# Optimization experiments

Measured on AMD Instinct MI355X. Metric: run time of the kernel, lower is better.

## Reference

```python
import jax, jax.numpy as jnp
import numpy as np

D = 1024      # d_model
H = 16        # heads
DH = D // H   # d_per_head = 64
E = 2         # expand_ratio
EPS = 1e-10


def _ln(x, g, b, eps=1e-5):
    mu = jnp.mean(x, axis=-1, keepdims=True)
    var = jnp.mean((x - mu) ** 2, axis=-1, keepdims=True)
    return (x - mu) / jnp.sqrt(var + eps) * g + b


def setup_inputs() -> dict:
    key = jax.random.key(0)
    ks = jax.random.split(key, 12)

    def w(k, fan_in, shape):
        return jax.random.normal(k, shape, jnp.float32) * (1.0 / np.sqrt(fan_in))

    return {
        "x": jax.random.normal(ks[0], (8, 1024, D), jnp.float32),
        "w_qvk": w(ks[1], D, (D, 3 * D)), "b_qvk": jnp.zeros((3 * D,), jnp.float32),
        "w_q": w(ks[2], D, (D, D)), "b_q": jnp.zeros((D,), jnp.float32),
        "w_k": w(ks[3], D, (D, D)), "b_k": jnp.zeros((D,), jnp.float32),
        "w_v": w(ks[4], D, (D, D)), "b_v": jnp.zeros((D,), jnp.float32),
        "w_o": w(ks[5], D, (D, D)), "b_o": jnp.zeros((D,), jnp.float32),
        "ln1_g": jnp.ones((D,), jnp.float32), "ln1_b": jnp.zeros((D,), jnp.float32),
        "w1": w(ks[6], D, (D, E * D)), "b1": jnp.zeros((E * D,), jnp.float32),
        "w2": w(ks[7], E * D, (E * D, D)), "b2": jnp.zeros((D,), jnp.float32),
        "ln2_g": jnp.ones((D,), jnp.float32), "ln2_b": jnp.zeros((D,), jnp.float32),
    }


def reference(x, w_qvk, b_qvk, w_q, b_q, w_k, b_k, w_v, b_v, w_o, b_o,
              ln1_g, ln1_b, w1, b1, w2, b2, ln2_g, ln2_b):
    n, m, _ = x.shape
    qvk = x @ w_qvk + b_qvk                       # [n, m, 3D]
    q = qvk[..., 0:D] @ w_q + b_q
    k = qvk[..., D:2 * D] @ w_k + b_k
    v = qvk[..., 2 * D:3 * D] @ w_v + b_v
    # NOTE: original rearranges '(d h)' with h=head -> head is the INNER factor
    q = q.reshape(n, m, DH, H)
    k = k.reshape(n, m, DH, H)
    v = v.reshape(n, m, DH, H)
    scores = jnp.einsum('nqdh,nkdh->nhqk', q, k) / (np.sqrt(DH) + EPS)
    p = jax.nn.softmax(scores, axis=-1)           # [n, h, q, k]
    vh = jnp.einsum('nkdh,nhqk->nhqd', v, p)      # [n, h, q, d]
    vh = vh.transpose(0, 2, 1, 3).reshape(n, m, D)  # 'n h q d -> n q (h d)'
    att = _ln(vh @ w_o + b_o, ln1_g, ln1_b)
    hidden = jnp.clip(att @ w1 + b1, 0.0, 6.0)    # ReLU6
    out = hidden @ w2 + b2
    return _ln(out, ln2_g, ln2_b)
```

## Files before the change

kernel.cpp:

```cpp
#include <hip/hip_runtime.h>
#include <math.h>


#define D_MODEL 1024
#define SEQ     1024
#define NHEAD   16

typedef short          s16x8 __attribute__((ext_vector_type(8)));
typedef unsigned short u16x4 __attribute__((ext_vector_type(4)));
typedef float          f32x4 __attribute__((ext_vector_type(4)));

__device__ __forceinline__ unsigned short f2bf(float f) {
    union { float f; unsigned u; } c; c.f = f;
    unsigned u = c.u;
    return (unsigned short)((u + 0x7FFFu + ((u >> 16) & 1u)) >> 16);
}
__device__ __forceinline__ float bf2f(unsigned short h) {
    union { unsigned u; float f; } c; c.u = ((unsigned)h) << 16; return c.f;
}

#define GLB(p) ((const __attribute__((address_space(1))) void*)(p))
#define LDSP(p) ((__attribute__((address_space(3))) void*)(p))

__global__ __launch_bounds__(256) void cast_f32_bf16(
    const float* __restrict__ in, unsigned short* __restrict__ out, int n4)
{
    int i = blockIdx.x * 256 + threadIdx.x;
    if (i < n4) {
        float4 v = ((const float4*)in)[i];
        u16x4 o;
        o[0] = f2bf(v.x); o[1] = f2bf(v.y); o[2] = f2bf(v.z); o[3] = f2bf(v.w);
        ((u16x4*)out)[i] = o;
    }
}

template <bool PERM>
__global__ __launch_bounds__(256) void wt_cast(
    const float* __restrict__ W, unsigned short* __restrict__ Wt, int K, int N)
{
    __shared__ float T[32][33];
    const int tx = threadIdx.x, ty = threadIdx.y;
    const int nb = blockIdx.x * 32, kb = blockIdx.y * 32;
    const int nOut = nb + tx;
    const int nSrc = PERM ? (((nOut & 63) << 4) + (nOut >> 6)) : nOut;
#pragma unroll
    for (int q = 0; q < 4; ++q)
        T[ty + q * 8][tx] = W[(size_t)(kb + ty + q * 8) * N + nSrc];
    __syncthreads();
#pragma unroll
    for (int q = 0; q < 4; ++q)
        Wt[(size_t)(nb + ty + q * 8) * K + kb + tx] = f2bf(T[tx][ty + q * 8]);
}

__global__ void perm_bias(const float* __restrict__ in, float* __restrict__ out)
{
    int i = threadIdx.x;
    out[i] = in[((i & 63) << 4) + (i >> 6)];
}

__global__ __launch_bounds__(256) void transpose_v(
    const unsigned short* __restrict__ vb, unsigned short* __restrict__ vt, int M)
{
    const int T = blockIdx.x * 256 + threadIdx.x;
    const int c  = T & 1023;
    const int r0 = (T >> 10) << 3;
    s16x8 o;
#pragma unroll
    for (int i = 0; i < 8; ++i)
        o[i] = (short)vb[(size_t)(r0 + i) * 1024 + c];
    *(s16x8*)&vt[(size_t)c * M + r0] = o;
}

template <int ACT>
__global__ __launch_bounds__(256) void gemm_bf16(
    const unsigned short* __restrict__ A, int lda,
    const unsigned short* __restrict__ Bt,
    const float* __restrict__ bias,
    unsigned short* __restrict__ C, int ldc,
    int M, int N, int K)
{
    __shared__ unsigned short At[128 * 32];
    __shared__ unsigned short Bl[128 * 32];
    const int tid = threadIdx.x;
    const int w = tid >> 6, l = tid & 63, g = l >> 4, lr = l & 15;
    const int row0 = blockIdx.y * 128, col0 = blockIdx.x * 128;
    const int wr = (w >> 1) * 64, wc = (w & 1) * 64;

    f32x4 zero = {0.f, 0.f, 0.f, 0.f};
    f32x4 acc[4][4];
#pragma unroll
    for (int m = 0; m < 4; ++m)
#pragma unroll
        for (int n = 0; n < 4; ++n) acc[m][n] = zero;

    const int srow = w * 32 + (l >> 2);
    const int scol = (l & 3) * 8;
    const unsigned short* aS = A + (size_t)(row0 + srow) * lda + scol;
    const unsigned short* bS = Bt + (size_t)(col0 + srow) * K + scol;
    unsigned short* aD0 = &At[w * 1024];
    unsigned short* aD1 = &At[w * 1024 + 512];
    unsigned short* bD0 = &Bl[w * 1024];
    unsigned short* bD1 = &Bl[w * 1024 + 512];

    for (int k0 = 0; k0 < K; k0 += 32) {
        __syncthreads();
        __builtin_amdgcn_global_load_lds(GLB(aS + k0), LDSP(aD0), 16, 0, 0);
        __builtin_amdgcn_global_load_lds(GLB(aS + (size_t)16 * lda + k0), LDSP(aD1), 16, 0, 0);
        __builtin_amdgcn_global_load_lds(GLB(bS + k0), LDSP(bD0), 16, 0, 0);
        __builtin_amdgcn_global_load_lds(GLB(bS + (size_t)16 * K + k0), LDSP(bD1), 16, 0, 0);
        __syncthreads();

        s16x8 a[4], b[4];
#pragma unroll
        for (int m = 0; m < 4; ++m)
            a[m] = *(const s16x8*)&At[(wr + m * 16 + lr) * 32 + g * 8];
#pragma unroll
        for (int n = 0; n < 4; ++n)
            b[n] = *(const s16x8*)&Bl[(wc + n * 16 + lr) * 32 + g * 8];
#pragma unroll
        for (int m = 0; m < 4; ++m)
#pragma unroll
            for (int n = 0; n < 4; ++n)
                acc[m][n] = __builtin_amdgcn_mfma_f32_16x16x32_bf16(
                    a[m], b[n], acc[m][n], 0, 0, 0);
    }

    float bv[4];
#pragma unroll
    for (int n = 0; n < 4; ++n) bv[n] = bias[col0 + wc + n * 16 + lr];
#pragma unroll
    for (int m = 0; m < 4; ++m)
#pragma unroll
        for (int n = 0; n < 4; ++n)
#pragma unroll
            for (int r = 0; r < 4; ++r) {
                float vv = acc[m][n][r] + bv[n];
                if (ACT == 1) vv = fminf(fmaxf(vv, 0.f), 6.f);
                const int row = row0 + wr + m * 16 + g * 4 + r;
                const int col = col0 + wc + n * 16 + lr;
                C[(size_t)row * ldc + col] = f2bf(vv);
            }
}

__global__ __launch_bounds__(256) void attn_mfma(
    const unsigned short* __restrict__ q,
    const unsigned short* __restrict__ k,
    const unsigned short* __restrict__ vt,
    unsigned short* __restrict__ vh, int M)
{
    __shared__ unsigned short Kt[64 * 64];
    __shared__ unsigned short Vl[64 * 64];
    __shared__ unsigned short Pt[4][16 * 64];

    const int tid = threadIdx.x, w = tid >> 6, l = tid & 63;
    const int g = l >> 4, lr = l & 15;
    const int qt = blockIdx.x, h = blockIdx.y, nb = blockIdx.z;

    const unsigned short* qB = q + (size_t)nb * SEQ * D_MODEL + h * 64;
    const unsigned short* kB = k + (size_t)nb * SEQ * D_MODEL + h * 64;
    const unsigned short* vB = vt + (size_t)h * 64 * M + nb * SEQ;

    s16x8 qa0, qa1;
    {
        const unsigned short* qp = qB + (size_t)(qt * 64 + w * 16 + lr) * D_MODEL + g * 8;
        qa0 = *(const s16x8*)qp;
        qa1 = *(const s16x8*)(qp + 32);
    }

    f32x4 zero = {0.f, 0.f, 0.f, 0.f};
    f32x4 Oc[4];
#pragma unroll
    for (int nd = 0; nd < 4; ++nd) Oc[nd] = zero;
    float mrun[4], lrun[4];
#pragma unroll
    for (int r = 0; r < 4; ++r) { mrun[r] = -3.0e38f; lrun[r] = 0.f; }

    const int srow = w * 16 + (l >> 3);
    const int scol = (((l & 7) * 16) ^ (((l >> 3) & 7) << 4)) >> 1;

    for (int kt = 0; kt < 16; ++kt) {
        __syncthreads();
        const unsigned short* ks0 = kB + (size_t)(kt * 64 + srow) * D_MODEL + scol;
        __builtin_amdgcn_global_load_lds(GLB(ks0), LDSP(&Kt[w * 1024]), 16, 0, 0);
        __builtin_amdgcn_global_load_lds(GLB(ks0 + (size_t)8 * D_MODEL),
                                         LDSP(&Kt[w * 1024 + 512]), 16, 0, 0);
        const unsigned short* vs0 = vB + (size_t)srow * M + kt * 64 + scol;
        __builtin_amdgcn_global_load_lds(GLB(vs0), LDSP(&Vl[w * 1024]), 16, 0, 0);
        __builtin_amdgcn_global_load_lds(GLB(vs0 + (size_t)8 * M),
                                         LDSP(&Vl[w * 1024 + 512]), 16, 0, 0);
        __syncthreads();

        f32x4 sc[4];
#pragma unroll
        for (int nk = 0; nk < 4; ++nk) {
            const int row = nk * 16 + lr;
            const int swz = (row & 7) << 4;
            const s16x8 b0 = *(const s16x8*)&Kt[row * 64 + (((g * 16) ^ swz) >> 1)];
            const s16x8 b1 = *(const s16x8*)&Kt[row * 64 + (((g * 16 + 64) ^ swz) >> 1)];
            sc[nk] = __builtin_amdgcn_mfma_f32_16x16x32_bf16(qa0, b0, zero, 0, 0, 0);
            sc[nk] = __builtin_amdgcn_mfma_f32_16x16x32_bf16(qa1, b1, sc[nk], 0, 0, 0);
        }

        float corr[4];
#pragma unroll
        for (int r = 0; r < 4; ++r) {
            float s0 = sc[0][r] * 0.125f, s1 = sc[1][r] * 0.125f;
            float s2 = sc[2][r] * 0.125f, s3 = sc[3][r] * 0.125f;
            float mt = fmaxf(fmaxf(s0, s1), fmaxf(s2, s3));
            mt = fmaxf(mt, __shfl_xor(mt, 1, 64));
            mt = fmaxf(mt, __shfl_xor(mt, 2, 64));
            mt = fmaxf(mt, __shfl_xor(mt, 4, 64));
            mt = fmaxf(mt, __shfl_xor(mt, 8, 64));
            const float mn = fmaxf(mrun[r], mt);
            corr[r] = __expf(mrun[r] - mn);
            mrun[r] = mn;
            float p0 = __expf(s0 - mn), p1 = __expf(s1 - mn);
            float p2 = __expf(s2 - mn), p3 = __expf(s3 - mn);
            float ps = p0 + p1 + p2 + p3;
            ps += __shfl_xor(ps, 1, 64);
            ps += __shfl_xor(ps, 2, 64);
            ps += __shfl_xor(ps, 4, 64);
            ps += __shfl_xor(ps, 8, 64);
            lrun[r] = lrun[r] * corr[r] + ps;

            const int qrow = g * 4 + r;
            const int pswz = (qrow & 7) << 4;
            Pt[w][qrow * 64 + (((2 * (0 * 16 + lr)) ^ pswz) >> 1)] = f2bf(p0);
            Pt[w][qrow * 64 + (((2 * (1 * 16 + lr)) ^ pswz) >> 1)] = f2bf(p1);
            Pt[w][qrow * 64 + (((2 * (2 * 16 + lr)) ^ pswz) >> 1)] = f2bf(p2);
            Pt[w][qrow * 64 + (((2 * (3 * 16 + lr)) ^ pswz) >> 1)] = f2bf(p3);
        }
#pragma unroll
        for (int nd = 0; nd < 4; ++nd)
#pragma unroll
            for (int r = 0; r < 4; ++r) Oc[nd][r] *= corr[r];

#pragma unroll
        for (int kk = 0; kk < 2; ++kk) {
            const int prswz = (lr & 7) << 4;
            const s16x8 pa = *(const s16x8*)
                &Pt[w][lr * 64 + (((g * 16 + kk * 64) ^ prswz) >> 1)];
#pragma unroll
            for (int nd = 0; nd < 4; ++nd) {
                const int row = nd * 16 + lr;
                const int vswz = (row & 7) << 4;
                const s16x8 bv = *(const s16x8*)
                    &Vl[row * 64 + (((g * 16 + kk * 64) ^ vswz) >> 1)];
                Oc[nd] = __builtin_amdgcn_mfma_f32_16x16x32_bf16(pa, bv, Oc[nd], 0, 0, 0);
            }
        }
    }

    float inv[4];
#pragma unroll
    for (int r = 0; r < 4; ++r) inv[r] = 1.0f / lrun[r];
#pragma unroll
    for (int nd = 0; nd < 4; ++nd)
#pragma unroll
        for (int r = 0; r < 4; ++r) {
            const int qrow = g * 4 + r;
            const int pswz = (qrow & 7) << 4;
            Pt[w][qrow * 64 + (((2 * (nd * 16 + lr)) ^ pswz) >> 1)] =
                f2bf(Oc[nd][r] * inv[r]);
        }
    const int rr = l >> 2;
    unsigned short* dst = vh + (size_t)(nb * SEQ + qt * 64 + w * 16 + rr) * D_MODEL + h * 64;
#pragma unroll
    for (int hh = 0; hh < 2; ++hh) {
        const int sb = (l & 3) * 32 + hh * 16;
        s16x8 o = *(const s16x8*)&Pt[w][rr * 64 + ((sb ^ ((rr & 7) << 4)) >> 1)];
        *(s16x8*)(dst + (sb >> 1)) = o;
    }
}

template <int OUTF32>
__global__ __launch_bounds__(256) void ln_bf16(
    const unsigned short* __restrict__ x,
    const float* __restrict__ gg,
    const float* __restrict__ bb,
    void* __restrict__ outp)
{
    const int row = blockIdx.x, tid = threadIdx.x;
    u16x4 xv = *(const u16x4*)&x[(size_t)row * 1024 + tid * 4];
    float f0 = bf2f(xv[0]), f1 = bf2f(xv[1]), f2 = bf2f(xv[2]), f3 = bf2f(xv[3]);
    float s  = f0 + f1 + f2 + f3;
    float sq = f0 * f0 + f1 * f1 + f2 * f2 + f3 * f3;
#pragma unroll
    for (int off = 1; off < 64; off <<= 1) {
        s  += __shfl_xor(s,  off, 64);
        sq += __shfl_xor(sq, off, 64);
    }
    __shared__ float ls[4], lq[4];
    const int wave = tid >> 6;
    if ((tid & 63) == 0) { ls[wave] = s; lq[wave] = sq; }
    __syncthreads();
    s  = ls[0] + ls[1] + ls[2] + ls[3];
    sq = lq[0] + lq[1] + lq[2] + lq[3];
    const float mu  = s * (1.0f / 1024.0f);
    const float var = sq * (1.0f / 1024.0f) - mu * mu;
    const float rs  = rsqrtf(var + 1e-5f);
    const float4 gv = ((const float4*)gg)[tid];
    const float4 bv = ((const float4*)bb)[tid];
    float o0 = (f0 - mu) * rs * gv.x + bv.x;
    float o1 = (f1 - mu) * rs * gv.y + bv.y;
    float o2 = (f2 - mu) * rs * gv.z + bv.z;
    float o3 = (f3 - mu) * rs * gv.w + bv.w;
    if (OUTF32) {
        float4 o; o.x = o0; o.y = o1; o.z = o2; o.w = o3;
        ((float4*)outp)[(size_t)row * 256 + tid] = o;
    } else {
        u16x4 o;
        o[0] = f2bf(o0); o[1] = f2bf(o1); o[2] = f2bf(o2); o[3] = f2bf(o3);
        ((u16x4*)outp)[(size_t)row * 256 + tid] = o;
    }
}

extern "C" void kernel_launch(void* const* d_in, const int* in_sizes, int n_in,
                              void* d_out, int out_size, void* d_ws, size_t ws_size,
                              hipStream_t stream)
{
    const float* x     = (const float*)d_in[0];
    const float* w_qvk = (const float*)d_in[1];
    const float* b_qvk = (const float*)d_in[2];
    const float* w_q   = (const float*)d_in[3];
    const float* b_q   = (const float*)d_in[4];
    const float* w_k   = (const float*)d_in[5];
    const float* b_k   = (const float*)d_in[6];
    const float* w_v   = (const float*)d_in[7];
    const float* b_v   = (const float*)d_in[8];
    const float* w_o   = (const float*)d_in[9];
    const float* b_o   = (const float*)d_in[10];
    const float* ln1_g = (const float*)d_in[11];
    const float* ln1_b = (const float*)d_in[12];
    const float* w1    = (const float*)d_in[13];
    const float* b1    = (const float*)d_in[14];
    const float* w2    = (const float*)d_in[15];
    const float* b2    = (const float*)d_in[16];
    const float* ln2_g = (const float*)d_in[17];
    const float* ln2_b = (const float*)d_in[18];
    float* out = (float*)d_out;

    const int nbatch = in_sizes[0] / (SEQ * D_MODEL);
    const int M = nbatch * SEQ;

    char* ws = (char*)d_ws;
    size_t off = 0;
    auto alloc = [&](size_t bytes) { size_t o = off; off += (bytes + 255) & ~(size_t)255; return o; };
    const size_t XB   = alloc((size_t)M * 1024 * 2);
    const size_t WQVK = alloc((size_t)3072 * 1024 * 2);
    const size_t WQ   = alloc((size_t)1024 * 1024 * 2);
    const size_t WK   = alloc((size_t)1024 * 1024 * 2);
    const size_t WV   = alloc((size_t)1024 * 1024 * 2);
    const size_t WO   = alloc((size_t)1024 * 1024 * 2);
    const size_t W1   = alloc((size_t)2048 * 1024 * 2);
    const size_t W2   = alloc((size_t)2048 * 1024 * 2);
    const size_t BQP  = alloc(4096);
    const size_t BKP  = alloc(4096);
    const size_t BVP  = alloc(4096);
    const size_t QVKB = alloc((size_t)M * 3072 * 2);
    const size_t QBUF = alloc((size_t)M * 1024 * 2);
    const size_t KBUF = alloc((size_t)M * 1024 * 2);
    const size_t VBUF = alloc((size_t)M * 1024 * 2);
    const size_t VT   = alloc((size_t)M * 1024 * 2);
    const size_t VH   = QVKB;
    const size_t ATTP = QVKB + (size_t)M * 1024 * 2;
    const size_t ATT  = QVKB + (size_t)M * 2048 * 2;
    const size_t HID  = QBUF;
    const size_t OUTP = VBUF;

    unsigned short* xb   = (unsigned short*)(ws + XB);
    unsigned short* wqvk = (unsigned short*)(ws + WQVK);
    unsigned short* wq   = (unsigned short*)(ws + WQ);
    unsigned short* wk   = (unsigned short*)(ws + WK);
    unsigned short* wv   = (unsigned short*)(ws + WV);
    unsigned short* wo   = (unsigned short*)(ws + WO);
    unsigned short* wt1  = (unsigned short*)(ws + W1);
    unsigned short* wt2  = (unsigned short*)(ws + W2);
    float*          bqp  = (float*)(ws + BQP);
    float*          bkp  = (float*)(ws + BKP);
    float*          bvp  = (float*)(ws + BVP);
    unsigned short* qvkb = (unsigned short*)(ws + QVKB);
    unsigned short* qb   = (unsigned short*)(ws + QBUF);
    unsigned short* kb   = (unsigned short*)(ws + KBUF);
    unsigned short* vb   = (unsigned short*)(ws + VBUF);
    unsigned short* vtb  = (unsigned short*)(ws + VT);
    unsigned short* vhb  = (unsigned short*)(ws + VH);
    unsigned short* attp = (unsigned short*)(ws + ATTP);
    unsigned short* attb = (unsigned short*)(ws + ATT);
    unsigned short* hid  = (unsigned short*)(ws + HID);
    unsigned short* outp = (unsigned short*)(ws + OUTP);

    const dim3 tb(32, 8);

    cast_f32_bf16<<<(M * 1024 / 4 + 255) / 256, 256, 0, stream>>>(x, xb, M * 1024 / 4);
    wt_cast<false><<<dim3(96, 32), tb, 0, stream>>>(w_qvk, wqvk, 1024, 3072);
    wt_cast<true ><<<dim3(32, 32), tb, 0, stream>>>(w_q, wq, 1024, 1024);
    wt_cast<true ><<<dim3(32, 32), tb, 0, stream>>>(w_k, wk, 1024, 1024);
    wt_cast<true ><<<dim3(32, 32), tb, 0, stream>>>(w_v, wv, 1024, 1024);
    wt_cast<false><<<dim3(32, 32), tb, 0, stream>>>(w_o, wo, 1024, 1024);
    wt_cast<false><<<dim3(64, 32), tb, 0, stream>>>(w1, wt1, 1024, 2048);
    wt_cast<false><<<dim3(32, 64), tb, 0, stream>>>(w2, wt2, 2048, 1024);
    perm_bias<<<1, 1024, 0, stream>>>(b_q, bqp);
    perm_bias<<<1, 1024, 0, stream>>>(b_k, bkp);
    perm_bias<<<1, 1024, 0, stream>>>(b_v, bvp);

    gemm_bf16<0><<<dim3(24, M / 128), 256, 0, stream>>>(
        xb, 1024, wqvk, b_qvk, qvkb, 3072, M, 3072, 1024);
    gemm_bf16<0><<<dim3(8, M / 128), 256, 0, stream>>>(
        qvkb + 0,    3072, wq, bqp, qb, 1024, M, 1024, 1024);
    gemm_bf16<0><<<dim3(8, M / 128), 256, 0, stream>>>(
        qvkb + 1024, 3072, wk, bkp, kb, 1024, M, 1024, 1024);
    gemm_bf16<0><<<dim3(8, M / 128), 256, 0, stream>>>(
        qvkb + 2048, 3072, wv, bvp, vb, 1024, M, 1024, 1024);

    transpose_v<<<(M / 8) * 1024 / 256, 256, 0, stream>>>(vb, vtb, M);
    attn_mfma<<<dim3(SEQ / 64, NHEAD, nbatch), 256, 0, stream>>>(qb, kb, vtb, vhb, M);

    gemm_bf16<0><<<dim3(8, M / 128), 256, 0, stream>>>(
        vhb, 1024, wo, b_o, attp, 1024, M, 1024, 1024);
    ln_bf16<0><<<M, 256, 0, stream>>>(attp, ln1_g, ln1_b, attb);

    gemm_bf16<1><<<dim3(16, M / 128), 256, 0, stream>>>(
        attb, 1024, wt1, b1, hid, 2048, M, 2048, 1024);
    gemm_bf16<0><<<dim3(8, M / 128), 256, 0, stream>>>(
        hid, 2048, wt2, b2, outp, 1024, M, 1024, 2048);
    ln_bf16<1><<<M, 256, 0, stream>>>(outp, ln2_g, ln2_b, out);
}
```

Before: 627.4 us.

## Fold chained QKV projections into combined weights and fold softmax scale

Precomputes the combined weight W_qvk_slice·W_q (and likewise for k and v) plus folded biases with a small weight-only MFMA GEMM, so activations pass through one 3072-wide GEMM instead of a QVK GEMM followed by three further 1024-wide GEMMs. The 1/sqrt(dh) scale is folded into the Q weights and bias, removing the per-score multiply in attention, and attention reads Q/K directly from the strided combined buffer. Softmax probabilities are converted with packed bf16 conversion instructions. This removes roughly 3 of 6 GFLOP-equivalents of activation GEMM work at the cost of a 3×1024³ weight GEMM per call and different rounding, since the combined weight is rounded to bf16 once.

```diff
diff --git a/kernel.cpp b/kernel.cpp
--- a/kernel.cpp
+++ b/kernel.cpp
@@ -52,14 +52,107 @@
         Wt[(size_t)(nb + ty + q * 8) * K + kb + tx] = f2bf(T[tx][ty + q * 8]);
 }
 
-__global__ void perm_bias(const float* __restrict__ in, float* __restrict__ out)
-{
-    int i = threadIdx.x;
-    out[i] = in[((i & 63) << 4) + (i >> 6)];
+__global__ __launch_bounds__(256) void bias_fold(
+    const float* __restrict__ bqvk,
+    const float* __restrict__ wq, const float* __restrict__ wk,
+    const float* __restrict__ wv,
+    const float* __restrict__ bq, const float* __restrict__ bk,
+    const float* __restrict__ bv,
+    float* __restrict__ bc)
+{
+    const int n  = blockIdx.x;
+    const int sl = blockIdx.y;
+    const float* w  = sl == 0 ? wq : sl == 1 ? wk : wv;
+    const float* bs = sl == 0 ? bq : sl == 1 ? bk : bv;
+    const int s = sl << 10;
+    const int nSrc = ((n & 63) << 4) + (n >> 6);
+    const int t = threadIdx.x;
+    float p = 0.f;
+    for (int k = t; k < 1024; k += 256)
+        p += bqvk[s + k] * w[(size_t)k * 1024 + nSrc];
+#pragma unroll
+    for (int off = 1; off < 64; off <<= 1) p += __shfl_xor(p, off, 64);
+    __shared__ float red[4];
+    if ((t & 63) == 0) red[t >> 6] = p;
+    __syncthreads();
+    if (t == 0) {
+        float dot = red[0] + red[1] + red[2] + red[3];
+        bc[s + n] = (dot + bs[nSrc]) * (sl == 0 ? 0.125f : 1.0f);
+    }
+}
+
+__global__ __launch_bounds__(256) void wcomb_mfma(
+    const unsigned short* __restrict__ Ws,
+    const unsigned short* __restrict__ Wb,
+    unsigned short* __restrict__ Wc)
+{
+    __shared__ unsigned short At[128 * 32];
+    __shared__ unsigned short Bl[128 * 32];
+    const int tid = threadIdx.x;
+    const int w = tid >> 6, l = tid & 63, g = l >> 4, lr = l & 15;
+    const int row0 = blockIdx.y * 128, col0 = blockIdx.x * 128;
+    const int z = blockIdx.z;
+    const int wr = (w >> 1) * 64, wcq = (w & 1) * 64;
+    const float scl = (z == 0) ? 0.125f : 1.0f;
+
+    const unsigned short* A  = Ws + (size_t)z * 1024 * 1024;
+    const unsigned short* Bt = Wb + z * 1024;
+    unsigned short*       C  = Wc + (size_t)z * 1024 * 1024;
+
+    f32x4 zero = {0.f, 0.f, 0.f, 0.f};
+    f32x4 acc[4][4];
+#pragma unroll
+    for (int m = 0; m < 4; ++m)
+#pragma unroll
+        for (int n = 0; n < 4; ++n) acc[m][n] = zero;
+
+    const int srow = w * 32 + (l >> 2);
+    const int scol = (l & 3) * 8;
+    const unsigned short* aS = A + (size_t)(row0 + srow) * 1024 + scol;
+    const unsigned short* bS = Bt + (size_t)(col0 + srow) * 3072 + scol;
+    unsigned short* aD0 = &At[w * 1024];
+    unsigned short* aD1 = &At[w * 1024 + 512];
+    unsigned short* bD0 = &Bl[w * 1024];
+    unsigned short* bD1 = &Bl[w * 1024 + 512];
+
+    for (int k0 = 0; k0 < 1024; k0 += 32) {
+        __syncthreads();
+        __builtin_amdgcn_global_load_lds(GLB(aS + k0), LDSP(aD0), 16, 0, 0);
+        __builtin_amdgcn_global_load_lds(GLB(aS + (size_t)16 * 1024 + k0), LDSP(aD1), 16, 0, 0);
+        __builtin_amdgcn_global_load_lds(GLB(bS + k0), LDSP(bD0), 16, 0, 0);
+        __builtin_amdgcn_global_load_lds(GLB(bS + (size_t)16 * 3072 + k0), LDSP(bD1), 16, 0, 0);
+        __syncthreads();
+
+        s16x8 a[4], b[4];
+#pragma unroll
+        for (int m = 0; m < 4; ++m)
+            a[m] = *(const s16x8*)&At[(wr + m * 16 + lr) * 32 + g * 8];
+#pragma unroll
+        for (int n = 0; n < 4; ++n)
+            b[n] = *(const s16x8*)&Bl[(wcq + n * 16 + lr) * 32 + g * 8];
+#pragma unroll
+        for (int m = 0; m < 4; ++m)
+#pragma unroll
+            for (int n = 0; n < 4; ++n)
+                acc[m][n] = __builtin_amdgcn_mfma_f32_16x16x32_bf16(
+                    a[m], b[n], acc[m][n], 0, 0, 0);
+    }
+
+#pragma unroll
+    for (int m = 0; m < 4; ++m)
+#pragma unroll
+        for (int n = 0; n < 4; ++n)
+#pragma unroll
+            for (int r = 0; r < 4; ++r) {
+                const int row = row0 + wr + m * 16 + g * 4 + r;
+                const int col = col0 + wcq + n * 16 + lr;
+                C[(size_t)row * 1024 + col] = f2bf(acc[m][n][r] * scl);
+            }
 }
 
 __global__ __launch_bounds__(256) void transpose_v(
-    const unsigned short* __restrict__ vb, unsigned short* __restrict__ vt, int M)
+    const unsigned short* __restrict__ vb, unsigned short* __restrict__ vt,
+    int M, int ldv)
 {
     const int T = blockIdx.x * 256 + threadIdx.x;
     const int c  = T & 1023;
@@ -67,7 +160,7 @@
     s16x8 o;
 #pragma unroll
     for (int i = 0; i < 8; ++i)
-        o[i] = (short)vb[(size_t)(r0 + i) * 1024 + c];
+        o[i] = (short)vb[(size_t)(r0 + i) * ldv + c];
     *(s16x8*)&vt[(size_t)c * M + r0] = o;
 }
 
@@ -143,10 +236,9 @@
 }
 
 __global__ __launch_bounds__(256) void attn_mfma(
-    const unsigned short* __restrict__ q,
-    const unsigned short* __restrict__ k,
+    const unsigned short* __restrict__ qkv,
     const unsigned short* __restrict__ vt,
-    unsigned short* __restrict__ vh, int M)
+    unsigned short* __restrict__ vh, int M, int ldq)
 {
     __shared__ unsigned short Kt[64 * 64];
     __shared__ unsigned short Vl[64 * 64];
@@ -156,13 +248,13 @@
     const int g = l >> 4, lr = l & 15;
     const int qt = blockIdx.x, h = blockIdx.y, nb = blockIdx.z;
 
-    const unsigned short* qB = q + (size_t)nb * SEQ * D_MODEL + h * 64;
-    const unsigned short* kB = k + (size_t)nb * SEQ * D_MODEL + h * 64;
+    const unsigned short* qB = qkv + (size_t)nb * SEQ * ldq + h * 64;
+    const unsigned short* kB = qkv + (size_t)nb * SEQ * ldq + 1024 + h * 64;
     const unsigned short* vB = vt + (size_t)h * 64 * M + nb * SEQ;
 
     s16x8 qa0, qa1;
     {
-        const unsigned short* qp = qB + (size_t)(qt * 64 + w * 16 + lr) * D_MODEL + g * 8;
+        const unsigned short* qp = qB + (size_t)(qt * 64 + w * 16 + lr) * ldq + g * 8;
         qa0 = *(const s16x8*)qp;
         qa1 = *(const s16x8*)(qp + 32);
     }
@@ -180,9 +272,9 @@
 
     for (int kt = 0; kt < 16; ++kt) {
         __syncthreads();
-        const unsigned short* ks0 = kB + (size_t)(kt * 64 + srow) * D_MODEL + scol;
+        const unsigned short* ks0 = kB + (size_t)(kt * 64 + srow) * ldq + scol;
         __builtin_amdgcn_global_load_lds(GLB(ks0), LDSP(&Kt[w * 1024]), 16, 0, 0);
-        __builtin_amdgcn_global_load_lds(GLB(ks0 + (size_t)8 * D_MODEL),
+        __builtin_amdgcn_global_load_lds(GLB(ks0 + (size_t)8 * ldq),
                                          LDSP(&Kt[w * 1024 + 512]), 16, 0, 0);
         const unsigned short* vs0 = vB + (size_t)srow * M + kt * 64 + scol;
         __builtin_amdgcn_global_load_lds(GLB(vs0), LDSP(&Vl[w * 1024]), 16, 0, 0);
@@ -204,8 +296,7 @@
         float corr[4];
 #pragma unroll
         for (int r = 0; r < 4; ++r) {
-            float s0 = sc[0][r] * 0.125f, s1 = sc[1][r] * 0.125f;
-            float s2 = sc[2][r] * 0.125f, s3 = sc[3][r] * 0.125f;
+            float s0 = sc[0][r], s1 = sc[1][r], s2 = sc[2][r], s3 = sc[3][r];
             float mt = fmaxf(fmaxf(s0, s1), fmaxf(s2, s3));
             mt = fmaxf(mt, __shfl_xor(mt, 1, 64));
             mt = fmaxf(mt, __shfl_xor(mt, 2, 64));
@@ -223,12 +314,15 @@
             ps += __shfl_xor(ps, 8, 64);
             lrun[r] = lrun[r] * corr[r] + ps;
 
+            unsigned pk01, pk23;
+            asm("v_cvt_pk_bf16_f32 %0, %1, %2" : "=v"(pk01) : "v"(p0), "v"(p1));
+            asm("v_cvt_pk_bf16_f32 %0, %1, %2" : "=v"(pk23) : "v"(p2), "v"(p3));
             const int qrow = g * 4 + r;
             const int pswz = (qrow & 7) << 4;
-            Pt[w][qrow * 64 + (((2 * (0 * 16 + lr)) ^ pswz) >> 1)] = f2bf(p0);
-            Pt[w][qrow * 64 + (((2 * (1 * 16 + lr)) ^ pswz) >> 1)] = f2bf(p1);
-            Pt[w][qrow * 64 + (((2 * (2 * 16 + lr)) ^ pswz) >> 1)] = f2bf(p2);
-            Pt[w][qrow * 64 + (((2 * (3 * 16 + lr)) ^ pswz) >> 1)] = f2bf(p3);
+            Pt[w][qrow * 64 + (((2 * (0 * 16 + lr)) ^ pswz) >> 1)] = (unsigned short)pk01;
+            Pt[w][qrow * 64 + (((2 * (1 * 16 + lr)) ^ pswz) >> 1)] = (unsigned short)(pk01 >> 16);
+            Pt[w][qrow * 64 + (((2 * (2 * 16 + lr)) ^ pswz) >> 1)] = (unsigned short)pk23;
+            Pt[w][qrow * 64 + (((2 * (3 * 16 + lr)) ^ pswz) >> 1)] = (unsigned short)(pk23 >> 16);
         }
 #pragma unroll
         for (int nd = 0; nd < 4; ++nd)
@@ -346,75 +440,57 @@
     char* ws = (char*)d_ws;
     size_t off = 0;
     auto alloc = [&](size_t bytes) { size_t o = off; off += (bytes + 255) & ~(size_t)255; return o; };
-    const size_t XB   = alloc((size_t)M * 1024 * 2);
-    const size_t WQVK = alloc((size_t)3072 * 1024 * 2);
-    const size_t WQ   = alloc((size_t)1024 * 1024 * 2);
-    const size_t WK   = alloc((size_t)1024 * 1024 * 2);
-    const size_t WV   = alloc((size_t)1024 * 1024 * 2);
-    const size_t WO   = alloc((size_t)1024 * 1024 * 2);
-    const size_t W1   = alloc((size_t)2048 * 1024 * 2);
-    const size_t W2   = alloc((size_t)2048 * 1024 * 2);
-    const size_t BQP  = alloc(4096);
-    const size_t BKP  = alloc(4096);
-    const size_t BVP  = alloc(4096);
-    const size_t QVKB = alloc((size_t)M * 3072 * 2);
-    const size_t QBUF = alloc((size_t)M * 1024 * 2);
-    const size_t KBUF = alloc((size_t)M * 1024 * 2);
-    const size_t VBUF = alloc((size_t)M * 1024 * 2);
-    const size_t VT   = alloc((size_t)M * 1024 * 2);
-    const size_t VH   = QVKB;
-    const size_t ATTP = QVKB + (size_t)M * 1024 * 2;
-    const size_t ATT  = QVKB + (size_t)M * 2048 * 2;
-    const size_t HID  = QBUF;
-    const size_t OUTP = VBUF;
-
-    unsigned short* xb   = (unsigned short*)(ws + XB);
-    unsigned short* wqvk = (unsigned short*)(ws + WQVK);
-    unsigned short* wq   = (unsigned short*)(ws + WQ);
-    unsigned short* wk   = (unsigned short*)(ws + WK);
-    unsigned short* wv   = (unsigned short*)(ws + WV);
-    unsigned short* wo   = (unsigned short*)(ws + WO);
-    unsigned short* wt1  = (unsigned short*)(ws + W1);
-    unsigned short* wt2  = (unsigned short*)(ws + W2);
-    float*          bqp  = (float*)(ws + BQP);
-    float*          bkp  = (float*)(ws + BKP);
-    float*          bvp  = (float*)(ws + BVP);
-    unsigned short* qvkb = (unsigned short*)(ws + QVKB);
-    unsigned short* qb   = (unsigned short*)(ws + QBUF);
-    unsigned short* kb   = (unsigned short*)(ws + KBUF);
-    unsigned short* vb   = (unsigned short*)(ws + VBUF);
-    unsigned short* vtb  = (unsigned short*)(ws + VT);
-    unsigned short* vhb  = (unsigned short*)(ws + VH);
-    unsigned short* attp = (unsigned short*)(ws + ATTP);
-    unsigned short* attb = (unsigned short*)(ws + ATT);
-    unsigned short* hid  = (unsigned short*)(ws + HID);
-    unsigned short* outp = (unsigned short*)(ws + OUTP);
+    const size_t XB    = alloc((size_t)M * 1024 * 2);
+    const size_t QKVB  = alloc((size_t)M * 3072 * 2);
+    const size_t VT    = alloc((size_t)M * 1024 * 2);
+    const size_t VH    = alloc((size_t)M * 1024 * 2);
+    const size_t WQVKB = alloc((size_t)1024 * 3072 * 2);
+    const size_t WSUB  = alloc((size_t)3 * 1024 * 1024 * 2);
+    const size_t WC    = alloc((size_t)3 * 1024 * 1024 * 2);
+    const size_t WO    = alloc((size_t)1024 * 1024 * 2);
+    const size_t W1    = alloc((size_t)2048 * 1024 * 2);
+    const size_t W2    = alloc((size_t)2048 * 1024 * 2);
+    const size_t BC    = alloc(3072 * 4);
+    const size_t ATTP = QKVB;
+    const size_t ATTB = QKVB + (size_t)M * 1024 * 2;
+    const size_t OUTP = QKVB + (size_t)M * 2048 * 2;
+    const size_t HID  = VT;
+
+    unsigned short* xb    = (unsigned short*)(ws + XB);
+    unsigned short* qkvb  = (unsigned short*)(ws + QKVB);
+    unsigned short* vtb   = (unsigned short*)(ws + VT);
+    unsigned short* vhb   = (unsigned short*)(ws + VH);
+    unsigned short* wqvkb = (unsigned short*)(ws + WQVKB);
+    unsigned short* wsub  = (unsigned short*)(ws + WSUB);
+    unsigned short* wc    = (unsigned short*)(ws + WC);
+    unsigned short* wo    = (unsigned short*)(ws + WO);
+    unsigned short* wt1   = (unsigned short*)(ws + W1);
+    unsigned short* wt2   = (unsigned short*)(ws + W2);
+    float*          bc    = (float*)(ws + BC);
+    unsigned short* attp  = (unsigned short*)(ws + ATTP);
+    unsigned short* attb  = (unsigned short*)(ws + ATTB);
+    unsigned short* hid   = (unsigned short*)(ws + HID);
+    unsigned short* outp  = (unsigned short*)(ws + OUTP);
 
     const dim3 tb(32, 8);
 
     cast_f32_bf16<<<(M * 1024 / 4 + 255) / 256, 256, 0, stream>>>(x, xb, M * 1024 / 4);
-    wt_cast<false><<<dim3(96, 32), tb, 0, stream>>>(w_qvk, wqvk, 1024, 3072);
-    wt_cast<true ><<<dim3(32, 32), tb, 0, stream>>>(w_q, wq, 1024, 1024);
-    wt_cast<true ><<<dim3(32, 32), tb, 0, stream>>>(w_k, wk, 1024, 1024);
-    wt_cast<true ><<<dim3(32, 32), tb, 0, stream>>>(w_v, wv, 1024, 1024);
+    cast_f32_bf16<<<(1024 * 3072 / 4 + 255) / 256, 256, 0, stream>>>(w_qvk, wqvkb, 1024 * 3072 / 4);
+    wt_cast<true ><<<dim3(32, 32), tb, 0, stream>>>(w_q, wsub + 0 * 1024 * 1024, 1024, 1024);
+    wt_cast<true ><<<dim3(32, 32), tb, 0, stream>>>(w_k, wsub + 1 * 1024 * 1024, 1024, 1024);
+    wt_cast<true ><<<dim3(32, 32), tb, 0, stream>>>(w_v, wsub + 2 * 1024 * 1024, 1024, 1024);
     wt_cast<false><<<dim3(32, 32), tb, 0, stream>>>(w_o, wo, 1024, 1024);
     wt_cast<false><<<dim3(64, 32), tb, 0, stream>>>(w1, wt1, 1024, 2048);
     wt_cast<false><<<dim3(32, 64), tb, 0, stream>>>(w2, wt2, 2048, 1024);
-    perm_bias<<<1, 1024, 0, stream>>>(b_q, bqp);
-    perm_bias<<<1, 1024, 0, stream>>>(b_k, bkp);
-    perm_bias<<<1, 1024, 0, stream>>>(b_v, bvp);
+    bias_fold<<<dim3(1024, 3), 256, 0, stream>>>(b_qvk, w_q, w_k, w_v,
+                                                 b_q, b_k, b_v, bc);
+    wcomb_mfma<<<dim3(8, 8, 3), 256, 0, stream>>>(wsub, wqvkb, wc);
 
     gemm_bf16<0><<<dim3(24, M / 128), 256, 0, stream>>>(
-        xb, 1024, wqvk, b_qvk, qvkb, 3072, M, 3072, 1024);
-    gemm_bf16<0><<<dim3(8, M / 128), 256, 0, stream>>>(
-        qvkb + 0,    3072, wq, bqp, qb, 1024, M, 1024, 1024);
-    gemm_bf16<0><<<dim3(8, M / 128), 256, 0, stream>>>(
-        qvkb + 1024, 3072, wk, bkp, kb, 1024, M, 1024, 1024);
-    gemm_bf16<0><<<dim3(8, M / 128), 256, 0, stream>>>(
-        qvkb + 2048, 3072, wv, bvp, vb, 1024, M, 1024, 1024);
-
-    transpose_v<<<(M / 8) * 1024 / 256, 256, 0, stream>>>(vb, vtb, M);
-    attn_mfma<<<dim3(SEQ / 64, NHEAD, nbatch), 256, 0, stream>>>(qb, kb, vtb, vhb, M);
+        xb, 1024, wc, bc, qkvb, 3072, M, 3072, 1024);
+
+    transpose_v<<<(M / 8) * 1024 / 256, 256, 0, stream>>>(qkvb + 2048, vtb, M, 3072);
+    attn_mfma<<<dim3(SEQ / 64, NHEAD, nbatch), 256, 0, stream>>>(qkvb, vtb, vhb, M, 3072);
 
     gemm_bf16<0><<<dim3(8, M / 128), 256, 0, stream>>>(
         vhb, 1024, wo, b_o, attp, 1024, M, 1024, 1024);
```

Measured after the change: 578.7 us. 7.8% less time.
